# Kernel tuning notes

Hardware: AMD Instinct MI355X
Metric: run time of the kernel (lower is better)

Reference implementation:

```python
import jax, jax.numpy as jnp
import numpy as np

DEPTH = 8
INPUT_WIDTH = 64
INNER_WIDTH = 32
BATCH = 65536
N_NODES = 2 ** DEPTH - 1   # 255 inner nodes
N_LEAVES = 2 ** DEPTH      # 256 bins
EPS = 1e-8


def _tree_paths(depth):
    """For each leaf, the inner-node index at each level and whether the path
    goes right (right child uses 1 - decision, mirroring hstack([p, 1-p]) indexing)."""
    node_idx = np.zeros((2 ** depth, depth), dtype=np.int32)
    is_right = np.zeros((2 ** depth, depth), dtype=bool)
    for leaf in range(2 ** depth):
        idx = 0
        for level in range(depth):
            bit = (leaf >> (depth - 1 - level)) & 1
            node_idx[leaf, level] = idx
            is_right[leaf, level] = bool(bit)
            idx = 2 * idx + 1 + bit
    return node_idx, is_right

_NODE_IDX_NP, _IS_RIGHT_NP = _tree_paths(DEPTH)
NODE_IDX = jnp.asarray(_NODE_IDX_NP)   # [L, depth]
IS_RIGHT = jnp.asarray(_IS_RIGHT_NP)   # [L, depth]


def _init_b_i():
    """Replicates PartialRadialLayer.init_tree_weights: thresholds evenly dividing [0,1],
    stored as logits so sigmoid(b_i) recovers the threshold."""
    b = np.zeros(N_NODES, dtype=np.float64)
    b[0] = -0.5
    used = 1
    for i in range(1, DEPTH):
        n_nodes = 2 ** i
        div = float(2 ** (i + 1))
        for node in range(n_nodes):
            b[used + node] = -(2 * node + 1) / div
        used += n_nodes
    return np.log(-b / (1.0 + b)).astype(np.float32).reshape(1, -1)


def setup_inputs() -> dict:
    key = jax.random.key(0)
    kx, kr, kt = jax.random.split(key, 3)
    x = jax.random.normal(kx, (BATCH, INPUT_WIDTH), dtype=jnp.float32)
    # kaiming_normal_ on [1, input_width]: fan_in = input_width
    ray = jax.random.normal(kr, (1, INPUT_WIDTH), dtype=jnp.float32) * np.sqrt(2.0 / INPUT_WIDTH)
    # kaiming_normal_ on [L, I, W]: fan_in = I * W
    inner_transforms = jax.random.normal(kt, (N_LEAVES, INPUT_WIDTH, INNER_WIDTH), dtype=jnp.float32) * np.sqrt(2.0 / (INPUT_WIDTH * INNER_WIDTH))
    w_i = jnp.zeros((1, N_NODES), dtype=jnp.float32)
    a_i = 5.0 * jnp.ones((1, N_NODES), dtype=jnp.float32)
    b_i = jnp.asarray(_init_b_i())
    return {"x": x, "ray": ray, "inner_transforms": inner_transforms,
            "w_i": w_i, "b_i": b_i, "a_i": a_i}


def reference(x, ray, inner_transforms, w_i, b_i, a_i):
    # angles: arccos(cosine_similarity(x, ray)) / pi
    x_norm = jnp.maximum(jnp.linalg.norm(x, axis=1), EPS)            # [B]
    r_norm = jnp.maximum(jnp.linalg.norm(ray, axis=1), EPS)          # [1]
    cos = jnp.clip((x @ ray[0]) / (x_norm * r_norm), -1.0, 1.0)      # [B]
    angles = jnp.arccos(cos) / jnp.pi                                # [B]

    # per-node decisions
    node_fns = (0.5 + jax.nn.sigmoid(w_i)) * angles[:, None] - jax.nn.sigmoid(b_i)  # [B, N]
    decisions = jax.nn.sigmoid(node_fns * (1.0 + a_i))                               # [B, N]

    # soft bin distribution: product along each root-to-leaf path
    g = decisions[:, NODE_IDX]                       # [B, L, depth]
    vals = jnp.where(IS_RIGHT, 1.0 - g, g)           # right child -> 1 - p
    distribution = jnp.prod(vals, axis=2)            # [B, L]

    # weighted per-leaf transforms: einsum('bi,liw->blw') then ('bl,blo->bo'), fused
    out = jnp.einsum('bl,bi,liw->bw', distribution, x, inner_transforms)
    return out
```

## Files before the change

kernel.cpp:

```cpp
#include <hip/hip_runtime.h>
#include <hip/hip_bf16.h>

#define NLEAF 256
#define MBLK 256
#define THREADS 512

typedef __attribute__((ext_vector_type(4))) float f32x4;
typedef __attribute__((ext_vector_type(4))) unsigned int uint4v;
typedef __attribute__((ext_vector_type(8))) __bf16 bf16x8;
typedef __attribute__((ext_vector_type(4))) __bf16 bf16x4;

#define OFF_DIST 0
#define OFF_XP   131072
#define OFF_T    147456
#define OFF_AC   155648
#define OFF_BC   156672
#define OFF_ANG  157696
#define OFF_RAY  158720
#define SMEM_BYTES 158976

__device__ __forceinline__ float sigf(float s) { return 1.0f / (1.0f + __expf(-s)); }

__global__ __launch_bounds__(256) void prep_T(const float* __restrict__ T,
                                              __bf16* __restrict__ wsT) {
  __shared__ char tile[4096];
  const int l = blockIdx.x;
  const float* src = T + (size_t)l * 2048;
  const int t = threadIdx.x;
#pragma unroll
  for (int p = 0; p < 2; ++p) {
    int e = p * 1024 + t * 4;
    f32x4 v = *(const f32x4*)(src + e);
    int k = e >> 5, w0 = e & 31;
#pragma unroll
    for (int j = 0; j < 4; ++j) {
      int w = w0 + j;
      int off = (w * 128 + 2 * k) ^ ((w & 7) << 4);
      *(__bf16*)(tile + off) = (__bf16)v[j];
    }
  }
  __syncthreads();
  *(uint4v*)((char*)wsT + (size_t)l * 4096 + t * 16) = *(const uint4v*)(tile + t * 16);
}

template <bool USE_WS>
__global__ __launch_bounds__(THREADS, 2)
void prl_main(const float* __restrict__ x, const float* __restrict__ ray,
              const float* __restrict__ w_i, const float* __restrict__ b_i,
              const float* __restrict__ a_i, const void* __restrict__ tsrc,
              float* __restrict__ out) {
  extern __shared__ char smem[];
  const int tid = threadIdx.x;
  const int lane = tid & 63;
  const int wid = tid >> 6;
  const int g = lane >> 4;
  const int ln = lane & 15;
  const int row0 = blockIdx.x * MBLK;

  float* A_c = (float*)(smem + OFF_AC);
  float* B_c = (float*)(smem + OFF_BC);
  float* angles = (float*)(smem + OFF_ANG);
  float* ray_l = (float*)(smem + OFF_RAY);
  __bf16* distb = (__bf16*)(smem + OFF_DIST);

  if (tid < 255) {
    float aa = 1.0f + a_i[tid];
    A_c[tid] = (0.5f + sigf(w_i[tid])) * aa;
    B_c[tid] = -sigf(b_i[tid]) * aa;
  }
  if (tid >= 256 && tid < 320) ray_l[tid - 256] = ray[tid - 256];
  __syncthreads();

  bf16x8 afrag[2][2] = {};
  float* xp = (float*)(smem + OFF_XP);
  for (int c = 0; c < 4; ++c) {
    const float* xg = x + (size_t)(row0 + c * 64) * 64;
#pragma unroll
    for (int p = 0; p < 2; ++p) {
      int idx = p * 512 + tid;
      f32x4 v = *(const f32x4*)(xg + idx * 4);
      *(f32x4*)(xp + idx * 4) = v;
      int cg = idx & 15;
      f32x4 rv = *(const f32x4*)(ray_l + cg * 4);
      float a0 = v[0] * v[0] + v[1] * v[1] + v[2] * v[2] + v[3] * v[3];
      float a1 = v[0] * rv[0] + v[1] * rv[1] + v[2] * rv[2] + v[3] * rv[3];
      float a2 = rv[0] * rv[0] + rv[1] * rv[1] + rv[2] * rv[2] + rv[3] * rv[3];
#pragma unroll
      for (int s = 1; s < 16; s <<= 1) {
        a0 += __shfl_xor(a0, s, 64);
        a1 += __shfl_xor(a1, s, 64);
        a2 += __shfl_xor(a2, s, 64);
      }
      if ((tid & 15) == 0) {
        int r = idx >> 4;
        float xn = fmaxf(sqrtf(a0), 1e-8f);
        float rn = fmaxf(sqrtf(a2), 1e-8f);
        float cs = a1 / (xn * rn);
        cs = fminf(fmaxf(cs, -1.0f), 1.0f);
        angles[c * 64 + r] = acosf(cs) * 0.31830988618379067f;
      }
    }
    __syncthreads();
    if ((wid >> 1) == c) {
#pragma unroll
      for (int mt = 0; mt < 2; ++mt)
#pragma unroll
        for (int kt = 0; kt < 2; ++kt) {
          int rl = (wid & 1) * 32 + mt * 16 + ln;
          int k0 = kt * 32 + g * 8;
          f32x4 u0 = *(const f32x4*)(xp + rl * 64 + k0);
          f32x4 u1 = *(const f32x4*)(xp + rl * 64 + k0 + 4);
          bf16x8 af;
          af[0] = (__bf16)u0[0]; af[1] = (__bf16)u0[1];
          af[2] = (__bf16)u0[2]; af[3] = (__bf16)u0[3];
          af[4] = (__bf16)u1[0]; af[5] = (__bf16)u1[1];
          af[6] = (__bf16)u1[2]; af[7] = (__bf16)u1[3];
          afrag[mt][kt] = af;
        }
    }
    __syncthreads();
  }

  __bf16* PA = (__bf16*)(smem + OFF_XP);
  __bf16* PB = (__bf16*)(smem + OFF_XP + 8192);
  if (tid < 256) {
    float ang = angles[tid];
    float d = sigf(fmaf(A_c[0], ang, B_c[0]));
    PA[tid] = (__bf16)d;
    PA[256 + tid] = (__bf16)(1.0f - d);
  }
  __syncthreads();
  {
    int n = tid >> 8, r = tid & 255;
    float p = (float)PA[tid];
    float ang = angles[r];
    float d = sigf(fmaf(A_c[1 + n], ang, B_c[1 + n]));
    PB[(2 * n) * 256 + r] = (__bf16)(p * d);
    PB[(2 * n + 1) * 256 + r] = (__bf16)(p * (1.0f - d));
  }
  __syncthreads();
#pragma unroll
  for (int it = 0; it < 2; ++it) {
    int e = it * 512 + tid;
    int n = e >> 8, r = e & 255;
    float p = (float)PB[e];
    float ang = angles[r];
    float d = sigf(fmaf(A_c[3 + n], ang, B_c[3 + n]));
    PA[(2 * n) * 256 + r] = (__bf16)(p * d);
    PA[(2 * n + 1) * 256 + r] = (__bf16)(p * (1.0f - d));
  }
  __syncthreads();
#pragma unroll
  for (int it = 0; it < 4; ++it) {
    int e = it * 512 + tid;
    int n = e >> 8, r = e & 255;
    float p = (float)PA[e];
    float ang = angles[r];
    float d = sigf(fmaf(A_c[7 + n], ang, B_c[7 + n]));
    PB[(2 * n) * 256 + r] = (__bf16)(p * d);
    PB[(2 * n + 1) * 256 + r] = (__bf16)(p * (1.0f - d));
  }
  __syncthreads();
#pragma unroll
  for (int it = 0; it < 8; ++it) {
    int e = it * 512 + tid;
    int n4 = e >> 8, r = e & 255;
    float p4 = (float)PB[e];
    float ang = angles[r];
    float d4 = sigf(fmaf(A_c[15 + n4], ang, B_c[15 + n4]));
    float p5[2] = {p4 * d4, p4 * (1.0f - d4)};
#pragma unroll
    for (int b5 = 0; b5 < 2; ++b5) {
      int n5 = 2 * n4 + b5;
      float d5 = sigf(fmaf(A_c[31 + n5], ang, B_c[31 + n5]));
      float p6[2] = {p5[b5] * d5, p5[b5] * (1.0f - d5)};
#pragma unroll
      for (int b6 = 0; b6 < 2; ++b6) {
        int n6 = 2 * n5 + b6;
        float d6 = sigf(fmaf(A_c[63 + n6], ang, B_c[63 + n6]));
        float p7[2] = {p6[b6] * d6, p6[b6] * (1.0f - d6)};
#pragma unroll
        for (int b7 = 0; b7 < 2; ++b7) {
          int n7 = 2 * n6 + b7;
          float d7 = sigf(fmaf(A_c[127 + n7], ang, B_c[127 + n7]));
          float pv = p7[b7];
          distb[(2 * n7) * 256 + r] = (__bf16)(pv * d7);
          distb[(2 * n7 + 1) * 256 + r] = (__bf16)(pv * (1.0f - d7));
        }
      }
    }
  }

  f32x4 acc[2][2] = {};
  const int strip = wid * 32;
  char* tb = smem + OFF_T;

  uint4v tv = {};
  f32x4 tvf = {};
  if constexpr (USE_WS) {
    if (tid < 256) {
      tv = *(const uint4v*)((const char*)tsrc + tid * 16);
      *(uint4v*)(tb + tid * 16) = tv;
      tv = *(const uint4v*)((const char*)tsrc + 4096 + tid * 16);
    }
  } else {
    tvf = *(const f32x4*)((const float*)tsrc + tid * 4);
    {
      int e4 = tid * 4, k = e4 >> 5, wb = e4 & 31;
#pragma unroll
      for (int j = 0; j < 4; ++j) {
        int w = wb + j;
        int ad = (w * 128 + 2 * k) ^ ((w & 7) << 4);
        *(__bf16*)(tb + ad) = (__bf16)tvf[j];
      }
    }
    tvf = *(const f32x4*)((const float*)tsrc + 2048 + tid * 4);
  }
  __syncthreads();

  for (int l = 0; l < NLEAF; ++l) {
    char* cur = tb + (l & 1) * 4096;
    char* nxt = tb + ((l + 1) & 1) * 4096;
    if constexpr (USE_WS) {
      if (tid < 256) {
        if (l + 1 < NLEAF) *(uint4v*)(nxt + tid * 16) = tv;
        if (l + 2 < NLEAF)
          tv = *(const uint4v*)((const char*)tsrc + (size_t)(l + 2) * 4096 + tid * 16);
      }
    } else {
      if (l + 1 < NLEAF) {
        int e4 = tid * 4, k = e4 >> 5, wb = e4 & 31;
#pragma unroll
        for (int j = 0; j < 4; ++j) {
          int w = wb + j;
          int ad = (w * 128 + 2 * k) ^ ((w & 7) << 4);
          *(__bf16*)(nxt + ad) = (__bf16)tvf[j];
        }
      }
      if (l + 2 < NLEAF)
        tvf = *(const f32x4*)((const float*)tsrc + (size_t)(l + 2) * 2048 + tid * 4);
    }
    f32x4 dv[2];
#pragma unroll
    for (int mt = 0; mt < 2; ++mt) {
      int row = strip + mt * 16 + g * 4;
      bf16x4 dd = *(const bf16x4*)(distb + l * 256 + row);
      dv[mt] = (f32x4){(float)dd[0], (float)dd[1], (float)dd[2], (float)dd[3]};
    }
    bf16x8 bfr[2][2];
#pragma unroll
    for (int kt = 0; kt < 2; ++kt)
#pragma unroll
      for (int nt = 0; nt < 2; ++nt) {
        int w = nt * 16 + ln;
        int ad = (w * 128 + kt * 64 + g * 16) ^ ((w & 7) << 4);
        bfr[kt][nt] = *(const bf16x8*)(cur + ad);
      }
    f32x4 zero = {0.0f, 0.0f, 0.0f, 0.0f};
#pragma unroll
    for (int mt = 0; mt < 2; ++mt)
#pragma unroll
      for (int nt = 0; nt < 2; ++nt) {
        f32x4 y = __builtin_amdgcn_mfma_f32_16x16x32_bf16(afrag[mt][0], bfr[0][nt], zero, 0, 0, 0);
        y = __builtin_amdgcn_mfma_f32_16x16x32_bf16(afrag[mt][1], bfr[1][nt], y, 0, 0, 0);
        acc[mt][nt] += dv[mt] * y;
      }
    __syncthreads();
  }

#pragma unroll
  for (int mt = 0; mt < 2; ++mt)
#pragma unroll
    for (int nt = 0; nt < 2; ++nt)
#pragma unroll
      for (int e = 0; e < 4; ++e) {
        int row = row0 + strip + mt * 16 + g * 4 + e;
        out[(size_t)row * 32 + nt * 16 + ln] = acc[mt][nt][e];
      }
}

extern "C" void kernel_launch(void* const* d_in, const int* in_sizes, int n_in,
                              void* d_out, int out_size, void* d_ws, size_t ws_size,
                              hipStream_t stream) {
  const float* x = (const float*)d_in[0];
  const float* ray = (const float*)d_in[1];
  const float* T = (const float*)d_in[2];
  const float* w_i = (const float*)d_in[3];
  const float* b_i = (const float*)d_in[4];
  const float* a_i = (const float*)d_in[5];
  float* out = (float*)d_out;

  bool use_ws = ws_size >= (size_t)NLEAF * 4096;
  if (use_ws) {
    hipFuncSetAttribute(reinterpret_cast<const void*>(&prl_main<true>),
                        hipFuncAttributeMaxDynamicSharedMemorySize, SMEM_BYTES);
    prep_T<<<256, 256, 0, stream>>>(T, (__bf16*)d_ws);
    prl_main<true><<<256, THREADS, SMEM_BYTES, stream>>>(x, ray, w_i, b_i, a_i, d_ws, out);
  } else {
    hipFuncSetAttribute(reinterpret_cast<const void*>(&prl_main<false>),
                        hipFuncAttributeMaxDynamicSharedMemorySize, SMEM_BYTES);
    prl_main<false><<<256, THREADS, SMEM_BYTES, stream>>>(x, ray, w_i, b_i, a_i, T, out);
  }
}
```

Measured before the change: 163.8 us.

## Load leaf weights straight into registers in MFMA fragment layout, dropping LDS staging

```diff
diff --git a/kernel.cpp b/kernel.cpp
--- a/kernel.cpp
+++ b/kernel.cpp
@@ -3,7 +3,7 @@
 
 #define NLEAF 256
 #define MBLK 256
-#define THREADS 512
+#define THREADS 256
 
 typedef __attribute__((ext_vector_type(4))) float f32x4;
 typedef __attribute__((ext_vector_type(4))) unsigned int uint4v;
@@ -12,12 +12,11 @@
 
 #define OFF_DIST 0
 #define OFF_XP   131072
-#define OFF_T    147456
-#define OFF_AC   155648
-#define OFF_BC   156672
-#define OFF_ANG  157696
-#define OFF_RAY  158720
-#define SMEM_BYTES 158976
+#define OFF_AC   147456
+#define OFF_BC   148480
+#define OFF_ANG  149504
+#define OFF_RAY  150528
+#define SMEM_BYTES 150784
 
 __device__ __forceinline__ float sigf(float s) { return 1.0f / (1.0f + __expf(-s)); }
 
@@ -35,7 +34,8 @@
 #pragma unroll
     for (int j = 0; j < 4; ++j) {
       int w = w0 + j;
-      int off = (w * 128 + 2 * k) ^ ((w & 7) << 4);
+      int off = ((k >> 5) * 2 + (w >> 4)) * 1024 +
+                (((k >> 3) & 3) * 16 + (w & 15)) * 16 + (k & 7) * 2;
       *(__bf16*)(tile + off) = (__bf16)v[j];
     }
   }
@@ -44,7 +44,7 @@
 }
 
 template <bool USE_WS>
-__global__ __launch_bounds__(THREADS, 2)
+__global__ __launch_bounds__(THREADS, 1)
 void prl_main(const float* __restrict__ x, const float* __restrict__ ray,
               const float* __restrict__ w_i, const float* __restrict__ b_i,
               const float* __restrict__ a_i, const void* __restrict__ tsrc,
@@ -68,16 +68,16 @@
     A_c[tid] = (0.5f + sigf(w_i[tid])) * aa;
     B_c[tid] = -sigf(b_i[tid]) * aa;
   }
-  if (tid >= 256 && tid < 320) ray_l[tid - 256] = ray[tid - 256];
-  __syncthreads();
-
-  bf16x8 afrag[2][2] = {};
+  if (tid < 64) ray_l[tid] = ray[tid];
+  __syncthreads();
+
+  bf16x8 afrag[4][2] = {};
   float* xp = (float*)(smem + OFF_XP);
   for (int c = 0; c < 4; ++c) {
     const float* xg = x + (size_t)(row0 + c * 64) * 64;
 #pragma unroll
-    for (int p = 0; p < 2; ++p) {
-      int idx = p * 512 + tid;
+    for (int p = 0; p < 4; ++p) {
+      int idx = p * 256 + tid;
       f32x4 v = *(const f32x4*)(xg + idx * 4);
       *(f32x4*)(xp + idx * 4) = v;
       int cg = idx & 15;
@@ -101,12 +101,12 @@
       }
     }
     __syncthreads();
-    if ((wid >> 1) == c) {
-#pragma unroll
-      for (int mt = 0; mt < 2; ++mt)
+    if (wid == c) {
+#pragma unroll
+      for (int mt = 0; mt < 4; ++mt)
 #pragma unroll
         for (int kt = 0; kt < 2; ++kt) {
-          int rl = (wid & 1) * 32 + mt * 16 + ln;
+          int rl = mt * 16 + ln;
           int k0 = kt * 32 + g * 8;
           f32x4 u0 = *(const f32x4*)(xp + rl * 64 + k0);
           f32x4 u1 = *(const f32x4*)(xp + rl * 64 + k0 + 4);
@@ -123,16 +123,18 @@
 
   __bf16* PA = (__bf16*)(smem + OFF_XP);
   __bf16* PB = (__bf16*)(smem + OFF_XP + 8192);
-  if (tid < 256) {
+  {
     float ang = angles[tid];
     float d = sigf(fmaf(A_c[0], ang, B_c[0]));
     PA[tid] = (__bf16)d;
     PA[256 + tid] = (__bf16)(1.0f - d);
   }
   __syncthreads();
-  {
-    int n = tid >> 8, r = tid & 255;
-    float p = (float)PA[tid];
+#pragma unroll
+  for (int it = 0; it < 2; ++it) {
+    int e = it * 256 + tid;
+    int n = e >> 8, r = e & 255;
+    float p = (float)PA[e];
     float ang = angles[r];
     float d = sigf(fmaf(A_c[1 + n], ang, B_c[1 + n]));
     PB[(2 * n) * 256 + r] = (__bf16)(p * d);
@@ -140,8 +142,8 @@
   }
   __syncthreads();
 #pragma unroll
-  for (int it = 0; it < 2; ++it) {
-    int e = it * 512 + tid;
+  for (int it = 0; it < 4; ++it) {
+    int e = it * 256 + tid;
     int n = e >> 8, r = e & 255;
     float p = (float)PB[e];
     float ang = angles[r];
@@ -151,8 +153,8 @@
   }
   __syncthreads();
 #pragma unroll
-  for (int it = 0; it < 4; ++it) {
-    int e = it * 512 + tid;
+  for (int it = 0; it < 8; ++it) {
+    int e = it * 256 + tid;
     int n = e >> 8, r = e & 255;
     float p = (float)PA[e];
     float ang = angles[r];
@@ -162,8 +164,8 @@
   }
   __syncthreads();
 #pragma unroll
-  for (int it = 0; it < 8; ++it) {
-    int e = it * 512 + tid;
+  for (int it = 0; it < 16; ++it) {
+    int e = it * 256 + tid;
     int n4 = e >> 8, r = e & 255;
     float p4 = (float)PB[e];
     float ang = angles[r];
@@ -190,91 +192,89 @@
       }
     }
   }
-
-  f32x4 acc[2][2] = {};
-  const int strip = wid * 32;
-  char* tb = smem + OFF_T;
-
-  uint4v tv = {};
-  f32x4 tvf = {};
+  __syncthreads();
+
+  f32x4 acc[4][2] = {};
+  const char* bp = (const char*)tsrc + lane * 16;
+
+  auto step = [&](const bf16x8 (&bv)[4], int l) {
+    f32x4 dv[4];
+#pragma unroll
+    for (int mt = 0; mt < 4; ++mt) {
+      bf16x4 dd = *(const bf16x4*)(distb + l * 256 + wid * 64 + mt * 16 + g * 4);
+      dv[mt] = (f32x4){(float)dd[0], (float)dd[1], (float)dd[2], (float)dd[3]};
+    }
+    f32x4 zero = {0.0f, 0.0f, 0.0f, 0.0f};
+#pragma unroll
+    for (int mt = 0; mt < 4; ++mt)
+#pragma unroll
+      for (int nt = 0; nt < 2; ++nt) {
+        bf16x8 bk0, bk1;
+        if constexpr (USE_WS) {
+          bk0 = bv[nt];
+          bk1 = bv[2 + nt];
+        } else {
+          const float* tp0 = (const float*)tsrc + (size_t)l * 2048 + (g * 8) * 32 + nt * 16 + ln;
+          const float* tp1 = tp0 + 32 * 32;
+#pragma unroll
+          for (int j = 0; j < 8; ++j) {
+            bk0[j] = (__bf16)tp0[j * 32];
+            bk1[j] = (__bf16)tp1[j * 32];
+          }
+        }
+        f32x4 y = __builtin_amdgcn_mfma_f32_16x16x32_bf16(afrag[mt][0], bk0, zero, 0, 0, 0);
+        y = __builtin_amdgcn_mfma_f32_16x16x32_bf16(afrag[mt][1], bk1, y, 0, 0, 0);
+        acc[mt][nt] += dv[mt] * y;
+      }
+  };
+
   if constexpr (USE_WS) {
-    if (tid < 256) {
-      tv = *(const uint4v*)((const char*)tsrc + tid * 16);
-      *(uint4v*)(tb + tid * 16) = tv;
-      tv = *(const uint4v*)((const char*)tsrc + 4096 + tid * 16);
+    bf16x8 b0[4], b1[4], b2[4], b3[4];
+#pragma unroll
+    for (int f = 0; f < 4; ++f) {
+      b0[f] = *(const bf16x8*)(bp + 0 * 4096 + f * 1024);
+      b1[f] = *(const bf16x8*)(bp + 1 * 4096 + f * 1024);
+      b2[f] = *(const bf16x8*)(bp + 2 * 4096 + f * 1024);
+      b3[f] = *(const bf16x8*)(bp + 3 * 4096 + f * 1024);
+    }
+    for (int l = 0; l < NLEAF; l += 4) {
+      step(b0, l);
+      if (l + 4 < NLEAF) {
+        const char* q = bp + (size_t)(l + 4) * 4096;
+#pragma unroll
+        for (int f = 0; f < 4; ++f) b0[f] = *(const bf16x8*)(q + f * 1024);
+      }
+      step(b1, l + 1);
+      if (l + 5 < NLEAF) {
+        const char* q = bp + (size_t)(l + 5) * 4096;
+#pragma unroll
+        for (int f = 0; f < 4; ++f) b1[f] = *(const bf16x8*)(q + f * 1024);
+      }
+      step(b2, l + 2);
+      if (l + 6 < NLEAF) {
+        const char* q = bp + (size_t)(l + 6) * 4096;
+#pragma unroll
+        for (int f = 0; f < 4; ++f) b2[f] = *(const bf16x8*)(q + f * 1024);
+      }
+      step(b3, l + 3);
+      if (l + 7 < NLEAF) {
+        const char* q = bp + (size_t)(l + 7) * 4096;
+#pragma unroll
+        for (int f = 0; f < 4; ++f) b3[f] = *(const bf16x8*)(q + f * 1024);
+      }
     }
   } else {
-    tvf = *(const f32x4*)((const float*)tsrc + tid * 4);
-    {
-      int e4 = tid * 4, k = e4 >> 5, wb = e4 & 31;
-#pragma unroll
-      for (int j = 0; j < 4; ++j) {
-        int w = wb + j;
-        int ad = (w * 128 + 2 * k) ^ ((w & 7) << 4);
-        *(__bf16*)(tb + ad) = (__bf16)tvf[j];
-      }
-    }
-    tvf = *(const f32x4*)((const float*)tsrc + 2048 + tid * 4);
-  }
-  __syncthreads();
-
-  for (int l = 0; l < NLEAF; ++l) {
-    char* cur = tb + (l & 1) * 4096;
-    char* nxt = tb + ((l + 1) & 1) * 4096;
-    if constexpr (USE_WS) {
-      if (tid < 256) {
-        if (l + 1 < NLEAF) *(uint4v*)(nxt + tid * 16) = tv;
-        if (l + 2 < NLEAF)
-          tv = *(const uint4v*)((const char*)tsrc + (size_t)(l + 2) * 4096 + tid * 16);
-      }
-    } else {
-      if (l + 1 < NLEAF) {
-        int e4 = tid * 4, k = e4 >> 5, wb = e4 & 31;
-#pragma unroll
-        for (int j = 0; j < 4; ++j) {
-          int w = wb + j;
-          int ad = (w * 128 + 2 * k) ^ ((w & 7) << 4);
-          *(__bf16*)(nxt + ad) = (__bf16)tvf[j];
-        }
-      }
-      if (l + 2 < NLEAF)
-        tvf = *(const f32x4*)((const float*)tsrc + (size_t)(l + 2) * 2048 + tid * 4);
-    }
-    f32x4 dv[2];
-#pragma unroll
-    for (int mt = 0; mt < 2; ++mt) {
-      int row = strip + mt * 16 + g * 4;
-      bf16x4 dd = *(const bf16x4*)(distb + l * 256 + row);
-      dv[mt] = (f32x4){(float)dd[0], (float)dd[1], (float)dd[2], (float)dd[3]};
-    }
-    bf16x8 bfr[2][2];
-#pragma unroll
-    for (int kt = 0; kt < 2; ++kt)
-#pragma unroll
-      for (int nt = 0; nt < 2; ++nt) {
-        int w = nt * 16 + ln;
-        int ad = (w * 128 + kt * 64 + g * 16) ^ ((w & 7) << 4);
-        bfr[kt][nt] = *(const bf16x8*)(cur + ad);
-      }
-    f32x4 zero = {0.0f, 0.0f, 0.0f, 0.0f};
-#pragma unroll
-    for (int mt = 0; mt < 2; ++mt)
-#pragma unroll
-      for (int nt = 0; nt < 2; ++nt) {
-        f32x4 y = __builtin_amdgcn_mfma_f32_16x16x32_bf16(afrag[mt][0], bfr[0][nt], zero, 0, 0, 0);
-        y = __builtin_amdgcn_mfma_f32_16x16x32_bf16(afrag[mt][1], bfr[1][nt], y, 0, 0, 0);
-        acc[mt][nt] += dv[mt] * y;
-      }
-    __syncthreads();
-  }
-
-#pragma unroll
-  for (int mt = 0; mt < 2; ++mt)
+    bf16x8 dummy[4] = {};
+    for (int l = 0; l < NLEAF; ++l) step(dummy, l);
+  }
+
+#pragma unroll
+  for (int mt = 0; mt < 4; ++mt)
 #pragma unroll
     for (int nt = 0; nt < 2; ++nt)
 #pragma unroll
       for (int e = 0; e < 4; ++e) {
-        int row = row0 + strip + mt * 16 + g * 4 + e;
+        int row = row0 + wid * 64 + mt * 16 + g * 4 + e;
         out[(size_t)row * 32 + nt * 16 + ln] = acc[mt][nt][e];
       }
 }
```

After: 188.8 us. +15.2%, slower.
